# Kernel optimization log

Measured on AMD Instinct MI355X. Metric: run time of the kernel, lower is better.

Reference implementation:

```python
import jax, jax.numpy as jnp
import numpy as np

N_UAV = 4096      # number of agents (rows/cols of adjacency)
T = 3             # filter_length (hard-coded to 3 in the module)
FEAT = 36         # 4 cameras x 9 xys features per UAV per step
N_VIS = 6         # n_vis_out
H = 256           # hidden width; layer_sizes = [18, 256, 256, 256, 2]
D_IN = T * N_VIS  # 18
D_OUT = 2


def _lin_init(key, fan_in, fan_out):
    # torch.nn.Linear default: U(-1/sqrt(fan_in), 1/sqrt(fan_in))
    b = 1.0 / np.sqrt(fan_in)
    kw, kb = jax.random.split(key)
    W = jax.random.uniform(kw, (fan_in, fan_out), jnp.float32, -b, b)
    bias = jax.random.uniform(kb, (fan_out,), jnp.float32, -b, b)
    return W, bias


def setup_inputs() -> dict:
    key = jax.random.key(0)
    ks = jax.random.split(key, 8)
    W_vis, b_vis = _lin_init(ks[2], FEAT, N_VIS)
    W_h0, b_h0 = _lin_init(ks[3], D_IN, H)
    W_h1, b_h1 = _lin_init(ks[4], H, H)
    W_h2, b_h2 = _lin_init(ks[5], H, H)
    W_p, b_p = _lin_init(ks[6], H, D_OUT)
    return {
        "vis_feats": jax.random.normal(ks[0], (N_UAV, T, FEAT), jnp.float32),
        "a_nets": jax.random.uniform(ks[1], (N_UAV, N_UAV, T), jnp.float32),
        "W_vis": W_vis, "b_vis": b_vis,
        "W_h0": W_h0, "b_h0": b_h0,
        "W_h1": W_h1, "b_h1": b_h1,
        "W_h2": W_h2, "b_h2": b_h2,
        "W_p": W_p, "b_p": b_p,
    }


def reference(vis_feats, a_nets, W_vis, b_vis, W_h0, b_h0, W_h1, b_h1,
              W_h2, b_h2, W_p, b_p):
    n = vis_feats.shape[0]
    n_vis = W_vis.shape[1]
    t_steps = a_nets.shape[2]
    x_agg = jnp.zeros((n, t_steps * n_vis), vis_feats.dtype)  # [N, 18]
    for t in range(t_steps):  # fixed small loop (filter_length = 3)
        a = a_nets[:, :, t]                       # [N, N]
        x = vis_feats[:, t, :] @ W_vis + b_vis    # vis_predict -> [N, 6]
        # x * a_net.unsqueeze(2) summed over dim 1 == a_net @ x
        msg = a @ x                               # [N, 6]
        # x_agg[:, :-6].unsqueeze(1).repeat(1,N,1) * a_net_comm summed over
        # dim 1 == x_agg[:, :-6] * rowsum(a_net)
        tail = x_agg[:, :-n_vis] * jnp.sum(a, axis=1, keepdims=True)  # [N, 12]
        x_agg = jnp.concatenate([msg, tail], axis=1)  # [N, 18]
    u = jax.nn.relu(x_agg @ W_h0 + b_h0)
    u = jax.nn.relu(u @ W_h1 + b_h1)
    u = jax.nn.relu(u @ W_h2 + b_h2)
    u = u @ W_p + b_p
    return (x_agg, u)
```

## Files before the change

kernel.cpp:

```cpp
#include <hip/hip_runtime.h>
#include <hip/hip_bf16.h>

#define N 4096
#define TSTEPS 3
#define FEAT 36
#define NVIS 6
#define HID 256
#define DIN 18
#define DOUT 2

#define JT 512

typedef __attribute__((ext_vector_type(8))) short bf16x8;
typedef __attribute__((ext_vector_type(4))) float f32x4;

__device__ __forceinline__ short f2bf(float f) {
    unsigned u = __builtin_bit_cast(unsigned, f);
    unsigned r = (u + 0x7FFFu + ((u >> 16) & 1u)) >> 16;
    return (short)r;
}

__device__ __forceinline__ int srow(int r) {
    return (r >> 5) * 672 + (r & 31) * 20 + ((r >> 2) & 7) * 4;
}

__global__ void k_vis(const float* __restrict__ vis, const float* __restrict__ Wv,
                      const float* __restrict__ bv, float* __restrict__ xall) {
    int o = blockIdx.x * blockDim.x + threadIdx.x;
    if (o >= N * DIN) return;
    int j  = o / DIN;
    int ct = o - j * DIN;
    int t  = ct / NVIS;
    int c  = ct - t * NVIS;
    const float* vrow = vis + (size_t)j * (TSTEPS * FEAT) + t * FEAT;
    float acc = bv[c];
#pragma unroll
    for (int f = 0; f < FEAT; ++f) acc += vrow[f] * Wv[f * NVIS + c];
    xall[o] = acc;
}

__global__ void k_msg(const float* __restrict__ a, const float* __restrict__ xall,
                      float* __restrict__ xagg) {
    __shared__ float xs[16 * 672];
    const int tid  = threadIdx.x;
    const int lane = tid & 63;
    const int wave = tid >> 6;
    const int row_base = blockIdx.x * 8 + wave * 2;

    const float* a0 = a + (size_t)row_base       * (N * 3);
    const float* a1 = a + (size_t)(row_base + 1) * (N * 3);

    float acc[2][3][6];
    float s[2][2];
#pragma unroll
    for (int r = 0; r < 2; ++r) {
#pragma unroll
        for (int t = 0; t < 3; ++t)
#pragma unroll
            for (int c = 0; c < 6; ++c) acc[r][t][c] = 0.f;
        s[r][0] = 0.f; s[r][1] = 0.f;
    }

    for (int tile = 0; tile < N / JT; ++tile) {
        const int tb = tile * JT;
        __syncthreads();
        for (int idx = tid; idx < JT * DIN; idx += 256) {
            int jj = idx / DIN;
            int c  = idx - jj * DIN;
            xs[srow(jj) + c] = xall[(size_t)(tb + jj) * DIN + c];
        }
        __syncthreads();

#pragma unroll
        for (int chunk = 0; chunk < JT / 256; ++chunk) {
            const int jj = chunk * 256 + lane * 4;
            const size_t jb = (size_t)(tb + jj) * 3;
            const float4* pa0 = (const float4*)(a0 + jb);
            const float4* pa1 = (const float4*)(a1 + jb);
            float4 u0 = pa0[0], u1 = pa0[1], u2 = pa0[2];
            float4 v0 = pa1[0], v1 = pa1[1], v2 = pa1[2];
            const float av0[4][3] = {{u0.x,u0.y,u0.z},{u0.w,u1.x,u1.y},
                                     {u1.z,u1.w,u2.x},{u2.y,u2.z,u2.w}};
            const float av1[4][3] = {{v0.x,v0.y,v0.z},{v0.w,v1.x,v1.y},
                                     {v1.z,v1.w,v2.x},{v2.y,v2.z,v2.w}};
#pragma unroll
            for (int q = 0; q < 4; ++q) {
                const float* xr = xs + srow(jj + q);
                float4 x0 = *(const float4*)(xr);
                float4 x1 = *(const float4*)(xr + 4);
                float4 x2 = *(const float4*)(xr + 8);
                float4 x3 = *(const float4*)(xr + 12);
                const float xv[18] = {x0.x,x0.y,x0.z,x0.w, x1.x,x1.y,x1.z,x1.w,
                                      x2.x,x2.y,x2.z,x2.w, x3.x,x3.y,x3.z,x3.w,
                                      xr[16], xr[17]};
#pragma unroll
                for (int t = 0; t < 3; ++t)
#pragma unroll
                    for (int c = 0; c < 6; ++c) {
                        acc[0][t][c] += av0[q][t] * xv[t*6+c];
                        acc[1][t][c] += av1[q][t] * xv[t*6+c];
                    }
                s[0][0] += av0[q][1]; s[0][1] += av0[q][2];
                s[1][0] += av1[q][1]; s[1][1] += av1[q][2];
            }
        }
    }

#pragma unroll
    for (int m = 1; m < 64; m <<= 1) {
#pragma unroll
        for (int r = 0; r < 2; ++r) {
#pragma unroll
            for (int t = 0; t < 3; ++t)
#pragma unroll
                for (int c = 0; c < 6; ++c)
                    acc[r][t][c] += __shfl_xor(acc[r][t][c], m, 64);
            s[r][0] += __shfl_xor(s[r][0], m, 64);
            s[r][1] += __shfl_xor(s[r][1], m, 64);
        }
    }

    if (lane == 0) {
#pragma unroll
        for (int r = 0; r < 2; ++r) {
            const float s1 = s[r][0], s2 = s[r][1];
            float* orow = xagg + (size_t)(row_base + r) * DIN;
#pragma unroll
            for (int c = 0; c < 6; ++c) {
                orow[c]      = acc[r][2][c];
                orow[6 + c]  = acc[r][1][c] * s2;
                orow[12 + c] = acc[r][0][c] * s1 * s2;
            }
        }
    }
}

__global__ void k_wprep(const float* __restrict__ W1, const float* __restrict__ W2,
                        short* __restrict__ Wp) {
    int t = blockIdx.x * 256 + threadIdx.x;
    int L  = t >> 16;
    int e  = t & 65535;
    int jj = e & 7;
    int l  = (e >> 3) & 63;
    int j  = (e >> 9) & 15;
    int s  = e >> 13;
    int k  = s * 32 + ((l >> 4) << 3) + jj;
    int n  = (j << 4) + (l & 15);
    const float* W = L ? W2 : W1;
    Wp[t] = f2bf(W[k * HID + n]);
}

__global__ void k_mlp_mfma(const float* __restrict__ xagg,
                           const float* __restrict__ W0, const float* __restrict__ b0,
                           const float* __restrict__ b1, const float* __restrict__ b2,
                           const short* __restrict__ Wp,
                           const float* __restrict__ Wpf, const float* __restrict__ bp,
                           float* __restrict__ u_out) {
    __shared__ float  xa[16][DIN];
    __shared__ short  hA[16 * 256];
    __shared__ short  hB[16 * 256];
    __shared__ float  h3[16 * 257];
    const int tid  = threadIdx.x;
    const int lane = tid & 63;
    const int wv   = tid >> 6;
    const int base = blockIdx.x * 16;

    for (int idx = tid; idx < 16 * DIN; idx += 256) {
        int r = idx / DIN, e = idx - r * DIN;
        xa[r][e] = xagg[(size_t)(base + r) * DIN + e];
    }
    __syncthreads();

    {
        const int g  = tid >> 5;
        const int n0 = (tid & 31) * 8;
        float acc[2][8];
#pragma unroll
        for (int jn = 0; jn < 8; ++jn) {
            float b = b0[n0 + jn];
            acc[0][jn] = b; acc[1][jn] = b;
        }
        for (int k = 0; k < DIN; ++k) {
            float4 wa = *(const float4*)&W0[k * HID + n0];
            float4 wb = *(const float4*)&W0[k * HID + n0 + 4];
            const float w[8] = {wa.x,wa.y,wa.z,wa.w, wb.x,wb.y,wb.z,wb.w};
            float xr0 = xa[2*g][k], xr1 = xa[2*g+1][k];
#pragma unroll
            for (int jn = 0; jn < 8; ++jn) {
                acc[0][jn] += xr0 * w[jn];
                acc[1][jn] += xr1 * w[jn];
            }
        }
#pragma unroll
        for (int r = 0; r < 2; ++r) {
            int row = 2 * g + r;
            bf16x8 v;
#pragma unroll
            for (int jn = 0; jn < 8; ++jn) v[jn] = f2bf(fmaxf(acc[r][jn], 0.f));
            *(bf16x8*)&hA[(row * 256 + n0) ^ ((row & 7) << 3)] = v;
        }
    }
    __syncthreads();

    const int arow = lane & 15;
    const int kgrp = (lane >> 4) << 3;
#pragma unroll 1
    for (int L = 0; L < 2; ++L) {
        const short* hsrc = L ? hB : hA;
        const float* bias = L ? b2 : b1;
        const short* WpL  = Wp + L * 65536;

        bf16x8 Af[8];
#pragma unroll
        for (int s = 0; s < 8; ++s)
            Af[s] = *(const bf16x8*)&hsrc[(arow * 256 + s * 32 + kgrp) ^ ((arow & 7) << 3)];

        f32x4 acc[4];
#pragma unroll
        for (int jt = 0; jt < 4; ++jt) {
            float b = bias[wv * 64 + jt * 16 + (lane & 15)];
            acc[jt] = (f32x4){b, b, b, b};
        }
#pragma unroll
        for (int s = 0; s < 8; ++s) {
#pragma unroll
            for (int jt = 0; jt < 4; ++jt) {
                int j = wv * 4 + jt;
                bf16x8 Bf = *(const bf16x8*)&WpL[(((s * 16 + j) * 64) + lane) * 8];
                acc[jt] = __builtin_amdgcn_mfma_f32_16x16x32_bf16(Af[s], Bf, acc[jt], 0, 0, 0);
            }
        }
        __syncthreads();
#pragma unroll
        for (int jt = 0; jt < 4; ++jt) {
            int n = wv * 64 + jt * 16 + (lane & 15);
#pragma unroll
            for (int q = 0; q < 4; ++q) {
                int row = ((lane >> 4) << 2) + q;
                float v = fmaxf(acc[jt][q], 0.f);
                if (L == 0) hB[(row * 256 + n) ^ ((row & 7) << 3)] = f2bf(v);
                else        h3[row * 257 + n] = v;
            }
        }
        __syncthreads();
    }

    {
        const int r  = tid >> 4;
        const int d  = (tid >> 3) & 1;
        const int ks = tid & 7;
        float acc = 0.f;
        const float* hr = &h3[r * 257 + ks * 32];
#pragma unroll
        for (int i = 0; i < 32; ++i) acc += hr[i] * Wpf[(ks * 32 + i) * DOUT + d];
        acc += __shfl_xor(acc, 1, 64);
        acc += __shfl_xor(acc, 2, 64);
        acc += __shfl_xor(acc, 4, 64);
        if (ks == 0) u_out[(size_t)(base + r) * DOUT + d] = acc + bp[d];
    }
}

#define HPITCH 20
__global__ __launch_bounds__(512, 2) void k_mlp(const float* __restrict__ xagg,
                      const float* __restrict__ W0, const float* __restrict__ b0,
                      const float* __restrict__ W1, const float* __restrict__ b1,
                      const float* __restrict__ W2, const float* __restrict__ b2,
                      const float* __restrict__ Wp, const float* __restrict__ bp,
                      float* __restrict__ u_out) {
    __shared__ float xa[16][DIN];
    __shared__ float hb[2][HID][HPITCH];
    const int tid   = threadIdx.x;
    const int n     = tid & 255;
    const int rbase = (tid >> 8) * 8;
    const int base  = blockIdx.x * 16;

    for (int idx = tid; idx < 16 * DIN; idx += 512) {
        int r = idx / DIN, e = idx - r * DIN;
        xa[r][e] = xagg[(size_t)(base + r) * DIN + e];
    }
    __syncthreads();
    {
        float accv[8];
#pragma unroll
        for (int r = 0; r < 8; ++r) accv[r] = b0[n];
        for (int k = 0; k < DIN; ++k) {
            float w = W0[k * HID + n];
#pragma unroll
            for (int r = 0; r < 8; ++r) accv[r] += xa[rbase + r][k] * w;
        }
#pragma unroll
        for (int r = 0; r < 8; ++r) hb[0][n][rbase + r] = fmaxf(accv[r], 0.f);
    }
    __syncthreads();
    {
        float accv[8];
#pragma unroll
        for (int r = 0; r < 8; ++r) accv[r] = b1[n];
        for (int k = 0; k < HID; ++k) {
            float w = W1[k * HID + n];
            const float4* hp = (const float4*)&hb[0][k][rbase];
            float4 h0 = hp[0], h1 = hp[1];
            const float hv[8] = {h0.x,h0.y,h0.z,h0.w, h1.x,h1.y,h1.z,h1.w};
#pragma unroll
            for (int r = 0; r < 8; ++r) accv[r] += hv[r] * w;
        }
#pragma unroll
        for (int r = 0; r < 8; ++r) hb[1][n][rbase + r] = fmaxf(accv[r], 0.f);
    }
    __syncthreads();
    {
        float accv[8];
#pragma unroll
        for (int r = 0; r < 8; ++r) accv[r] = b2[n];
        for (int k = 0; k < HID; ++k) {
            float w = W2[k * HID + n];
            const float4* hp = (const float4*)&hb[1][k][rbase];
            float4 h0 = hp[0], h1 = hp[1];
            const float hv[8] = {h0.x,h0.y,h0.z,h0.w, h1.x,h1.y,h1.z,h1.w};
#pragma unroll
            for (int r = 0; r < 8; ++r) accv[r] += hv[r] * w;
        }
#pragma unroll
        for (int r = 0; r < 8; ++r) hb[0][n][rbase + r] = fmaxf(accv[r], 0.f);
    }
    __syncthreads();
    if (tid < 32) {
        int r = tid >> 1, d = tid & 1;
        float acc = bp[d];
        for (int k = 0; k < HID; ++k) acc += hb[0][k][r] * Wp[k * DOUT + d];
        u_out[(size_t)(base + r) * DOUT + d] = acc;
    }
}

extern "C" void kernel_launch(void* const* d_in, const int* in_sizes, int n_in,
                              void* d_out, int out_size, void* d_ws, size_t ws_size,
                              hipStream_t stream) {
    const float* vis  = (const float*)d_in[0];
    const float* anet = (const float*)d_in[1];
    const float* Wv   = (const float*)d_in[2];
    const float* bv   = (const float*)d_in[3];
    const float* W0   = (const float*)d_in[4];
    const float* b0   = (const float*)d_in[5];
    const float* W1   = (const float*)d_in[6];
    const float* b1   = (const float*)d_in[7];
    const float* W2   = (const float*)d_in[8];
    const float* b2   = (const float*)d_in[9];
    const float* Wp   = (const float*)d_in[10];
    const float* bp   = (const float*)d_in[11];

    float* xagg  = (float*)d_out;
    float* u_out = (float*)d_out + (size_t)N*DIN;
    float* xall  = (float*)d_ws;
    short* Wpk   = (short*)((char*)d_ws + (512 << 10));

    k_vis<<<(N * DIN + 255) / 256, 256, 0, stream>>>(vis, Wv, bv, xall);
    k_msg<<<N / 8, 256, 0, stream>>>(anet, xall, xagg);

    if (ws_size >= (512 << 10) + 131072 * sizeof(short)) {
        k_wprep<<<512, 256, 0, stream>>>(W1, W2, Wpk);
        k_mlp_mfma<<<N / 16, 256, 0, stream>>>(xagg, W0, b0, b1, b2, Wpk, Wp, bp, u_out);
    } else {
        k_mlp<<<N / 16, 512, 0, stream>>>(xagg, W0, b0, W1, b1, W2, b2, Wp, bp, u_out);
    }
}
```

Measured before the change: 81.54 us.

## Fuse message aggregation with MFMA MLP and merge prep kernels

Folds the visual projection and the bf16 weight-packing into a single prep launch, split by block index. The message-passing kernel now keeps each block's 8 aggregated rows in shared memory, writes them out, and runs the three-layer MFMA MLP plus the output head directly. This cuts the launch count from four to two and removes the round trip of x_agg through global memory. In exchange, each MFMA tile now holds only 8 valid rows of 16, so half the matrix work is wasted, and the packed weights are fetched by twice as many blocks. Shared memory is reused through a union, which needs extra barriers.

```diff
diff --git a/kernel.cpp b/kernel.cpp
--- a/kernel.cpp
+++ b/kernel.cpp
@@ -1,5 +1,4 @@
 #include <hip/hip_runtime.h>
-#include <hip/hip_bf16.h>
 
 #define N 4096
 #define TSTEPS 3
@@ -24,28 +23,59 @@
     return (r >> 5) * 672 + (r & 31) * 20 + ((r >> 2) & 7) * 4;
 }
 
-__global__ void k_vis(const float* __restrict__ vis, const float* __restrict__ Wv,
-                      const float* __restrict__ bv, float* __restrict__ xall) {
-    int o = blockIdx.x * blockDim.x + threadIdx.x;
-    if (o >= N * DIN) return;
-    int j  = o / DIN;
-    int ct = o - j * DIN;
-    int t  = ct / NVIS;
-    int c  = ct - t * NVIS;
-    const float* vrow = vis + (size_t)j * (TSTEPS * FEAT) + t * FEAT;
-    float acc = bv[c];
-#pragma unroll
-    for (int f = 0; f < FEAT; ++f) acc += vrow[f] * Wv[f * NVIS + c];
-    xall[o] = acc;
-}
-
-__global__ void k_msg(const float* __restrict__ a, const float* __restrict__ xall,
-                      float* __restrict__ xagg) {
-    __shared__ float xs[16 * 672];
+__global__ void k_prep(const float* __restrict__ vis, const float* __restrict__ Wv,
+                       const float* __restrict__ bv, float* __restrict__ xall,
+                       const float* __restrict__ W1, const float* __restrict__ W2,
+                       short* __restrict__ Wp) {
+    if (blockIdx.x < 288) {
+        int o = blockIdx.x * 256 + threadIdx.x;
+        if (o >= N * DIN) return;
+        int j  = o / DIN;
+        int ct = o - j * DIN;
+        int t  = ct / NVIS;
+        int c  = ct - t * NVIS;
+        const float* vrow = vis + (size_t)j * (TSTEPS * FEAT) + t * FEAT;
+        float acc = bv[c];
+#pragma unroll
+        for (int f = 0; f < FEAT; ++f) acc += vrow[f] * Wv[f * NVIS + c];
+        xall[o] = acc;
+    } else {
+        int t = (blockIdx.x - 288) * 256 + threadIdx.x;
+        int L  = t >> 16;
+        int e  = t & 65535;
+        int jj = e & 7;
+        int l  = (e >> 3) & 63;
+        int j  = (e >> 9) & 15;
+        int s  = e >> 13;
+        int k  = s * 32 + ((l >> 4) << 3) + jj;
+        int n  = (j << 4) + (l & 15);
+        const float* W = L ? W2 : W1;
+        Wp[t] = f2bf(W[k * HID + n]);
+    }
+}
+
+template<int FUSE>
+__global__ void k_msg_mlp(const float* __restrict__ a, const float* __restrict__ xall,
+                          float* __restrict__ xagg,
+                          const short* __restrict__ Wp,
+                          const float* __restrict__ W0, const float* __restrict__ b0,
+                          const float* __restrict__ b1, const float* __restrict__ b2,
+                          const float* __restrict__ Wpf, const float* __restrict__ bp,
+                          float* __restrict__ u_out) {
+    __shared__ union SM {
+        float xs[16 * 672];
+        struct {
+            float xa[8][DIN];
+            short hA[16 * 256];
+            short hB[16 * 256];
+            float h3[16 * 257];
+        } m;
+    } sm;
     const int tid  = threadIdx.x;
     const int lane = tid & 63;
     const int wave = tid >> 6;
-    const int row_base = blockIdx.x * 8 + wave * 2;
+    const int row0 = blockIdx.x * 8;
+    const int row_base = row0 + wave * 2;
 
     const float* a0 = a + (size_t)row_base       * (N * 3);
     const float* a1 = a + (size_t)(row_base + 1) * (N * 3);
@@ -67,7 +97,7 @@
         for (int idx = tid; idx < JT * DIN; idx += 256) {
             int jj = idx / DIN;
             int c  = idx - jj * DIN;
-            xs[srow(jj) + c] = xall[(size_t)(tb + jj) * DIN + c];
+            sm.xs[srow(jj) + c] = xall[(size_t)(tb + jj) * DIN + c];
         }
         __syncthreads();
 
@@ -85,7 +115,7 @@
                                      {v1.z,v1.w,v2.x},{v2.y,v2.z,v2.w}};
 #pragma unroll
             for (int q = 0; q < 4; ++q) {
-                const float* xr = xs + srow(jj + q);
+                const float* xr = sm.xs + srow(jj + q);
                 float4 x0 = *(const float4*)(xr);
                 float4 x1 = *(const float4*)(xr + 4);
                 float4 x2 = *(const float4*)(xr + 8);
@@ -120,143 +150,105 @@
         }
     }
 
+    __syncthreads();
     if (lane == 0) {
 #pragma unroll
         for (int r = 0; r < 2; ++r) {
             const float s1 = s[r][0], s2 = s[r][1];
-            float* orow = xagg + (size_t)(row_base + r) * DIN;
+            float* xrow = sm.m.xa[wave * 2 + r];
 #pragma unroll
             for (int c = 0; c < 6; ++c) {
-                orow[c]      = acc[r][2][c];
-                orow[6 + c]  = acc[r][1][c] * s2;
-                orow[12 + c] = acc[r][0][c] * s1 * s2;
+                xrow[c]      = acc[r][2][c];
+                xrow[6 + c]  = acc[r][1][c] * s2;
+                xrow[12 + c] = acc[r][0][c] * s1 * s2;
             }
         }
     }
-}
-
-__global__ void k_wprep(const float* __restrict__ W1, const float* __restrict__ W2,
-                        short* __restrict__ Wp) {
-    int t = blockIdx.x * 256 + threadIdx.x;
-    int L  = t >> 16;
-    int e  = t & 65535;
-    int jj = e & 7;
-    int l  = (e >> 3) & 63;
-    int j  = (e >> 9) & 15;
-    int s  = e >> 13;
-    int k  = s * 32 + ((l >> 4) << 3) + jj;
-    int n  = (j << 4) + (l & 15);
-    const float* W = L ? W2 : W1;
-    Wp[t] = f2bf(W[k * HID + n]);
-}
-
-__global__ void k_mlp_mfma(const float* __restrict__ xagg,
-                           const float* __restrict__ W0, const float* __restrict__ b0,
-                           const float* __restrict__ b1, const float* __restrict__ b2,
-                           const short* __restrict__ Wp,
-                           const float* __restrict__ Wpf, const float* __restrict__ bp,
-                           float* __restrict__ u_out) {
-    __shared__ float  xa[16][DIN];
-    __shared__ short  hA[16 * 256];
-    __shared__ short  hB[16 * 256];
-    __shared__ float  h3[16 * 257];
-    const int tid  = threadIdx.x;
-    const int lane = tid & 63;
-    const int wv   = tid >> 6;
-    const int base = blockIdx.x * 16;
-
-    for (int idx = tid; idx < 16 * DIN; idx += 256) {
+    __syncthreads();
+
+    for (int idx = tid; idx < 8 * DIN; idx += 256) {
         int r = idx / DIN, e = idx - r * DIN;
-        xa[r][e] = xagg[(size_t)(base + r) * DIN + e];
-    }
-    __syncthreads();
+        xagg[(size_t)(row0 + r) * DIN + e] = sm.m.xa[r][e];
+    }
+
+    if (!FUSE) return;
 
     {
-        const int g  = tid >> 5;
-        const int n0 = (tid & 31) * 8;
-        float acc[2][8];
-#pragma unroll
-        for (int jn = 0; jn < 8; ++jn) {
-            float b = b0[n0 + jn];
-            acc[0][jn] = b; acc[1][jn] = b;
-        }
+        const int row = tid >> 5;
+        const int n0  = (tid & 31) * 8;
+        float accv[8];
+#pragma unroll
+        for (int jn = 0; jn < 8; ++jn) accv[jn] = b0[n0 + jn];
         for (int k = 0; k < DIN; ++k) {
             float4 wa = *(const float4*)&W0[k * HID + n0];
             float4 wb = *(const float4*)&W0[k * HID + n0 + 4];
             const float w[8] = {wa.x,wa.y,wa.z,wa.w, wb.x,wb.y,wb.z,wb.w};
-            float xr0 = xa[2*g][k], xr1 = xa[2*g+1][k];
-#pragma unroll
-            for (int jn = 0; jn < 8; ++jn) {
-                acc[0][jn] += xr0 * w[jn];
-                acc[1][jn] += xr1 * w[jn];
-            }
-        }
-#pragma unroll
-        for (int r = 0; r < 2; ++r) {
-            int row = 2 * g + r;
-            bf16x8 v;
-#pragma unroll
-            for (int jn = 0; jn < 8; ++jn) v[jn] = f2bf(fmaxf(acc[r][jn], 0.f));
-            *(bf16x8*)&hA[(row * 256 + n0) ^ ((row & 7) << 3)] = v;
-        }
+            float xr = sm.m.xa[row][k];
+#pragma unroll
+            for (int jn = 0; jn < 8; ++jn) accv[jn] += xr * w[jn];
+        }
+        bf16x8 v;
+#pragma unroll
+        for (int jn = 0; jn < 8; ++jn) v[jn] = f2bf(fmaxf(accv[jn], 0.f));
+        *(bf16x8*)&sm.m.hA[(row * 256 + n0) ^ ((row & 7) << 3)] = v;
     }
     __syncthreads();
 
     const int arow = lane & 15;
     const int kgrp = (lane >> 4) << 3;
+    const int wv   = wave;
 #pragma unroll 1
     for (int L = 0; L < 2; ++L) {
-        const short* hsrc = L ? hB : hA;
+        const short* hsrc = L ? sm.m.hB : sm.m.hA;
         const float* bias = L ? b2 : b1;
         const short* WpL  = Wp + L * 65536;
 
         bf16x8 Af[8];
 #pragma unroll
-        for (int s = 0; s < 8; ++s)
-            Af[s] = *(const bf16x8*)&hsrc[(arow * 256 + s * 32 + kgrp) ^ ((arow & 7) << 3)];
-
-        f32x4 acc[4];
+        for (int ks = 0; ks < 8; ++ks)
+            Af[ks] = *(const bf16x8*)&hsrc[(arow * 256 + ks * 32 + kgrp) ^ ((arow & 7) << 3)];
+
+        f32x4 c4[4];
 #pragma unroll
         for (int jt = 0; jt < 4; ++jt) {
             float b = bias[wv * 64 + jt * 16 + (lane & 15)];
-            acc[jt] = (f32x4){b, b, b, b};
-        }
-#pragma unroll
-        for (int s = 0; s < 8; ++s) {
+            c4[jt] = (f32x4){b, b, b, b};
+        }
+#pragma unroll
+        for (int ks = 0; ks < 8; ++ks) {
 #pragma unroll
             for (int jt = 0; jt < 4; ++jt) {
                 int j = wv * 4 + jt;
-                bf16x8 Bf = *(const bf16x8*)&WpL[(((s * 16 + j) * 64) + lane) * 8];
-                acc[jt] = __builtin_amdgcn_mfma_f32_16x16x32_bf16(Af[s], Bf, acc[jt], 0, 0, 0);
+                bf16x8 Bf = *(const bf16x8*)&WpL[(((ks * 16 + j) * 64) + lane) * 8];
+                c4[jt] = __builtin_amdgcn_mfma_f32_16x16x32_bf16(Af[ks], Bf, c4[jt], 0, 0, 0);
             }
         }
-        __syncthreads();
 #pragma unroll
         for (int jt = 0; jt < 4; ++jt) {
             int n = wv * 64 + jt * 16 + (lane & 15);
 #pragma unroll
             for (int q = 0; q < 4; ++q) {
                 int row = ((lane >> 4) << 2) + q;
-                float v = fmaxf(acc[jt][q], 0.f);
-                if (L == 0) hB[(row * 256 + n) ^ ((row & 7) << 3)] = f2bf(v);
-                else        h3[row * 257 + n] = v;
+                float v = fmaxf(c4[jt][q], 0.f);
+                if (L == 0) sm.m.hB[(row * 256 + n) ^ ((row & 7) << 3)] = f2bf(v);
+                else        sm.m.h3[row * 257 + n] = v;
             }
         }
         __syncthreads();
     }
 
-    {
+    if (tid < 128) {
         const int r  = tid >> 4;
         const int d  = (tid >> 3) & 1;
         const int ks = tid & 7;
-        float acc = 0.f;
-        const float* hr = &h3[r * 257 + ks * 32];
-#pragma unroll
-        for (int i = 0; i < 32; ++i) acc += hr[i] * Wpf[(ks * 32 + i) * DOUT + d];
-        acc += __shfl_xor(acc, 1, 64);
-        acc += __shfl_xor(acc, 2, 64);
-        acc += __shfl_xor(acc, 4, 64);
-        if (ks == 0) u_out[(size_t)(base + r) * DOUT + d] = acc + bp[d];
+        float accf = 0.f;
+        const float* hr = &sm.m.h3[r * 257 + ks * 32];
+#pragma unroll
+        for (int i = 0; i < 32; ++i) accf += hr[i] * Wpf[(ks * 32 + i) * DOUT + d];
+        accf += __shfl_xor(accf, 1, 64);
+        accf += __shfl_xor(accf, 2, 64);
+        accf += __shfl_xor(accf, 4, 64);
+        if (ks == 0) u_out[(size_t)(row0 + r) * DOUT + d] = accf + bp[d];
     }
 }
 
@@ -265,7 +257,7 @@
                       const float* __restrict__ W0, const float* __restrict__ b0,
                       const float* __restrict__ W1, const float* __restrict__ b1,
                       const float* __restrict__ W2, const float* __restrict__ b2,
-                      const float* __restrict__ Wp, const float* __restrict__ bp,
+                      const float* __restrict__ Wpf, const float* __restrict__ bp,
                       float* __restrict__ u_out) {
     __shared__ float xa[16][DIN];
     __shared__ float hb[2][HID][HPITCH];
@@ -327,7 +319,7 @@
     if (tid < 32) {
         int r = tid >> 1, d = tid & 1;
         float acc = bp[d];
-        for (int k = 0; k < HID; ++k) acc += hb[0][k][r] * Wp[k * DOUT + d];
+        for (int k = 0; k < HID; ++k) acc += hb[0][k][r] * Wpf[k * DOUT + d];
         u_out[(size_t)(base + r) * DOUT + d] = acc;
     }
 }
@@ -345,7 +337,7 @@
     const float* b1   = (const float*)d_in[7];
     const float* W2   = (const float*)d_in[8];
     const float* b2   = (const float*)d_in[9];
-    const float* Wp   = (const float*)d_in[10];
+    const float* Wpf  = (const float*)d_in[10];
     const float* bp   = (const float*)d_in[11];
 
     float* xagg  = (float*)d_out;
@@ -353,13 +345,16 @@
     float* xall  = (float*)d_ws;
     short* Wpk   = (short*)((char*)d_ws + (512 << 10));
 
-    k_vis<<<(N * DIN + 255) / 256, 256, 0, stream>>>(vis, Wv, bv, xall);
-    k_msg<<<N / 8, 256, 0, stream>>>(anet, xall, xagg);
-
-    if (ws_size >= (512 << 10) + 131072 * sizeof(short)) {
-        k_wprep<<<512, 256, 0, stream>>>(W1, W2, Wpk);
-        k_mlp_mfma<<<N / 16, 256, 0, stream>>>(xagg, W0, b0, b1, b2, Wpk, Wp, bp, u_out);
+    const bool fuse = ws_size >= (512 << 10) + 131072 * sizeof(short);
+
+    if (fuse) {
+        k_prep<<<800, 256, 0, stream>>>(vis, Wv, bv, xall, W1, W2, Wpk);
+        k_msg_mlp<1><<<N / 8, 256, 0, stream>>>(anet, xall, xagg, Wpk,
+                                                W0, b0, b1, b2, Wpf, bp, u_out);
     } else {
-        k_mlp<<<N / 16, 512, 0, stream>>>(xagg, W0, b0, W1, b1, W2, b2, Wp, bp, u_out);
-    }
-}
+        k_prep<<<288, 256, 0, stream>>>(vis, Wv, bv, xall, W1, W2, Wpk);
+        k_msg_mlp<0><<<N / 8, 256, 0, stream>>>(anet, xall, xagg, Wpk,
+                                                W0, b0, b1, b2, Wpf, bp, u_out);
+        k_mlp<<<N / 16, 512, 0, stream>>>(xagg, W0, b0, W1, b1, W2, b2, Wpf, bp, u_out);
+    }
+}
```

Result: faster. 75.54 us (-7.4%).
